# Kernel tuning notes

Measured on AMD Instinct MI355X. Metric: run time of the kernel, lower is better.

Reference implementation:

```python
import jax, jax.numpy as jnp
import numpy as np

HEADS = 4
DIM_HEAD = 32
SCALE = DIM_HEAD ** -0.5


def setup_inputs() -> dict:
    key = jax.random.key(0)
    k1, k2, k3 = jax.random.split(key, 3)
    B, C, H, W = 4, 128, 64, 64
    inner = HEADS * DIM_HEAD  # 128
    x = jax.random.normal(k1, (B, C, H, W), dtype=jnp.float32)
    # 1x1 conv weights == channel-mixing matrices [out_ch, in_ch]
    w_qkv = jax.random.normal(k2, (inner * 3, C), dtype=jnp.float32) * (C ** -0.5)
    w_proj = jax.random.normal(k3, (C, inner), dtype=jnp.float32) * (inner ** -0.5)
    b_proj = jnp.zeros((C,), dtype=jnp.float32)
    return {"x": x, "w_qkv": w_qkv, "w_proj": w_proj, "b_proj": b_proj}


def reference(x, w_qkv, w_proj, b_proj):
    b, c, h, w = x.shape
    n = h * w
    # 1x1 conv = per-pixel matmul over channels
    qkv = jnp.einsum('bchw,oc->bohw', x, w_qkv)  # [B, 3*inner, H, W]
    q, k, v = jnp.split(qkv, 3, axis=1)

    def to_heads(t):
        # [B, inner, H, W] -> [B, heads, HW, dim_head]
        return t.reshape(b, HEADS, DIM_HEAD, n).transpose(0, 1, 3, 2)

    q = to_heads(q) * SCALE
    k = to_heads(k)
    v = to_heads(v)
    # scores [B, heads, HW, HW]; softmax is max-stabilized (matches torch amax-subtract)
    scores = jnp.einsum('bhnd,bhmd->bhnm', q, k)
    attn = jax.nn.softmax(scores, axis=-1)
    out = jnp.einsum('bhnm,bhmd->bhnd', attn, v)  # [B, heads, HW, dim_head]
    out = out.transpose(0, 1, 3, 2).reshape(b, HEADS * DIM_HEAD, h, w)
    return jnp.einsum('bchw,oc->bohw', out, w_proj) + b_proj[None, :, None, None]
```

## Files before the change

### kernel.cpp

```cpp
#include <hip/hip_runtime.h>

typedef _Float16 f16;
typedef __attribute__((ext_vector_type(8))) f16 f16x8;
typedef __attribute__((ext_vector_type(4))) f16 f16x4;
typedef __attribute__((ext_vector_type(2))) __fp16 h16x2;
typedef __attribute__((ext_vector_type(4))) float floatx4;

#define NPIX 4096
#define KT   128
#define VROW 136
#define NSPLIT 4

__global__ __launch_bounds__(256) void cvt_w(
    const float* __restrict__ wq, const float* __restrict__ wp,
    f16* __restrict__ wh, f16* __restrict__ wph)
{
    const int idx = (blockIdx.x * 256 + threadIdx.x) * 4;
    const float qs = 0.17677669529663687f * 1.4426950408889634f;
    float4 v;
    f16* dst;
    if (idx < 49152) { v = *(const float4*)(wq + idx); dst = wh + idx; }
    else             { v = *(const float4*)(wp + (idx - 49152)); dst = wph + (idx - 49152); }
    if (idx < 16384) { v.x *= qs; v.y *= qs; v.z *= qs; v.w *= qs; }
    h16x2 a = __builtin_amdgcn_cvt_pkrtz(v.x, v.y);
    h16x2 b = __builtin_amdgcn_cvt_pkrtz(v.z, v.w);
    f16x4 h; h[0] = (f16)a[0]; h[1] = (f16)a[1]; h[2] = (f16)b[0]; h[3] = (f16)b[1];
    *(f16x4*)dst = h;
}

__global__ __launch_bounds__(256) void qkv_mfma(
    const float* __restrict__ x, const f16* __restrict__ wh,
    f16* __restrict__ qh, f16* __restrict__ kh, f16* __restrict__ vth)
{
    const int tid  = threadIdx.x;
    const int wave = tid >> 6;
    const int lane = tid & 63;
    const int quad = lane >> 4;
    const int l16  = lane & 15;
    const int pbase = blockIdx.x * 64;
    const int y     = blockIdx.y;
    const int b     = blockIdx.z;
    const int p_col = pbase + wave * 16 + l16;

    const float* xb = x + (size_t)b * 128 * NPIX;

    f16x8 xf[4];
#pragma unroll
    for (int kc = 0; kc < 4; ++kc) {
        const int c0 = kc * 32 + quad * 8;
        float e[8];
#pragma unroll
        for (int j = 0; j < 8; ++j)
            e[j] = xb[(size_t)(c0 + j) * NPIX + p_col];
#pragma unroll
        for (int j = 0; j < 4; ++j) {
            h16x2 pk = __builtin_amdgcn_cvt_pkrtz(e[2 * j], e[2 * j + 1]);
            xf[kc][2 * j] = (f16)pk[0]; xf[kc][2 * j + 1] = (f16)pk[1];
        }
    }

    floatx4 acc[4];
#pragma unroll
    for (int i = 0; i < 4; ++i) acc[i] = floatx4{0.f, 0.f, 0.f, 0.f};

    if (y < 4) {
#pragma unroll
        for (int n = 0; n < 4; ++n)
#pragma unroll
            for (int kc = 0; kc < 4; ++kc) {
                f16x8 wf = *(const f16x8*)&wh[(size_t)(y * 64 + n * 16 + l16) * 128 + kc * 32 + quad * 8];
                acc[n] = __builtin_amdgcn_mfma_f32_16x16x32_f16(xf[kc], wf, acc[n], 0, 0, 0);
            }
        f16* dst = (y < 2) ? qh : kh;
#pragma unroll
        for (int n = 0; n < 4; ++n) {
            const int og    = y * 64 + n * 16 + l16;
            const int local = og & 127;
            const int head  = local >> 5;
            const int d     = local & 31;
            f16* base = dst + (size_t)(b * 4 + head) * NPIX * 32;
#pragma unroll
            for (int r = 0; r < 4; ++r) {
                const int p = pbase + wave * 16 + quad * 4 + r;
                base[(size_t)p * 32 + d] = (f16)acc[n][r];
            }
        }
    } else {
#pragma unroll
        for (int m = 0; m < 4; ++m)
#pragma unroll
            for (int kc = 0; kc < 4; ++kc) {
                f16x8 wf = *(const f16x8*)&wh[(size_t)(y * 64 + m * 16 + l16) * 128 + kc * 32 + quad * 8];
                acc[m] = __builtin_amdgcn_mfma_f32_16x16x32_f16(wf, xf[kc], acc[m], 0, 0, 0);
            }
#pragma unroll
        for (int m = 0; m < 4; ++m)
#pragma unroll
            for (int r = 0; r < 4; ++r) {
                const int ov   = (y - 4) * 64 + m * 16 + quad * 4 + r;
                const int head = ov >> 5;
                const int d    = ov & 31;
                vth[((size_t)(b * 4 + head) * 32 + d) * NPIX + p_col] = (f16)acc[m][r];
            }
    }
}

__global__ __launch_bounds__(256, 4) void attn_kernel(
    const f16* __restrict__ qh, const f16* __restrict__ kh,
    const f16* __restrict__ vth, f16* __restrict__ po, float* __restrict__ pl)
{
    __shared__ f16 klds[KT * 32];
    __shared__ f16 vlds[32 * VROW];

    const int tid  = threadIdx.x;
    const int wave = tid >> 6;
    const int lane = tid & 63;
    const int quad = lane >> 4;
    const int l16  = lane & 15;

    const int n     = blockIdx.x;
    const int bh    = (n & 7) * 2 + ((n >> 3) & 1);
    const int qblk  = (n >> 4) & 31;
    const int split = (n >> 9) & 3;
    const int qbase = qblk * 128 + wave * 32;

    const f16* kb = kh + (size_t)bh * NPIX * 32;
    const f16* vb = vth + (size_t)bh * 32 * NPIX;

    f16x8 qB[2];
#pragma unroll
    for (int h = 0; h < 2; ++h)
        qB[h] = *(const f16x8*)(qh + ((size_t)bh * NPIX + qbase + h * 16 + l16) * 32 + quad * 8);

    f16x8 ones;
#pragma unroll
    for (int j = 0; j < 8; ++j) ones[j] = (l16 == 0) ? (f16)1.0f : (f16)0.0f;

    floatx4 oacc[2][2], lacc[2];
#pragma unroll
    for (int h = 0; h < 2; ++h) {
        lacc[h] = floatx4{0.f, 0.f, 0.f, 0.f};
#pragma unroll
        for (int dh = 0; dh < 2; ++dh) oacc[h][dh] = floatx4{0.f, 0.f, 0.f, 0.f};
    }

    for (int kt = split * 8; kt < split * 8 + 8; ++kt) {
        __syncthreads();
        {
            const int4* src = (const int4*)(kb + (size_t)kt * KT * 32);
            ((int4*)klds)[tid]       = src[tid];
            ((int4*)klds)[tid + 256] = src[tid + 256];
        }
        {
            const int r  = tid >> 3;
            const int cc = (tid & 7) * 2;
            const int4* vsrc = (const int4*)(vb + (size_t)r * NPIX + kt * KT + cc * 8);
            int4 v0 = vsrc[0], v1 = vsrc[1];
            int4* vdst = (int4*)(vlds + r * VROW + cc * 8);
            vdst[0] = v0; vdst[1] = v1;
        }
        __syncthreads();

        f16x8 kf[8];
#pragma unroll
        for (int t = 0; t < 8; ++t)
            kf[t] = *(const f16x8*)&klds[(t * 16 + l16) * 32 + quad * 8];

#pragma unroll
        for (int h = 0; h < 2; ++h) {
            floatx4 st[8];
            const floatx4 z0 = {0.f, 0.f, 0.f, 0.f};
#pragma unroll
            for (int t = 0; t < 8; ++t)
                st[t] = __builtin_amdgcn_mfma_f32_16x16x32_f16(kf[t], qB[h], z0, 0, 0, 0);

            f16x4 paf[8];
#pragma unroll
            for (int t = 0; t < 8; ++t) {
                float e0 = __builtin_amdgcn_exp2f(st[t][0]);
                float e1 = __builtin_amdgcn_exp2f(st[t][1]);
                float e2 = __builtin_amdgcn_exp2f(st[t][2]);
                float e3 = __builtin_amdgcn_exp2f(st[t][3]);
                h16x2 lo = __builtin_amdgcn_cvt_pkrtz(e0, e1);
                h16x2 hi = __builtin_amdgcn_cvt_pkrtz(e2, e3);
                paf[t][0] = (f16)lo[0]; paf[t][1] = (f16)lo[1];
                paf[t][2] = (f16)hi[0]; paf[t][3] = (f16)hi[1];
            }
#pragma unroll
            for (int g = 0; g < 4; ++g) {
                f16x8 pA;
#pragma unroll
                for (int j = 0; j < 4; ++j) { pA[j] = paf[2 * g][j]; pA[4 + j] = paf[2 * g + 1][j]; }
                lacc[h] = __builtin_amdgcn_mfma_f32_16x16x32_f16(pA, ones, lacc[h], 0, 0, 0);
#pragma unroll
                for (int dh = 0; dh < 2; ++dh) {
                    const f16* vrow = &vlds[(dh * 16 + l16) * VROW + 32 * g + quad * 4];
                    f16x4 v0 = *(const f16x4*)(vrow);
                    f16x4 v1 = *(const f16x4*)(vrow + 16);
                    f16x8 vB;
#pragma unroll
                    for (int j = 0; j < 4; ++j) { vB[j] = v0[j]; vB[4 + j] = v1[j]; }
                    oacc[h][dh] = __builtin_amdgcn_mfma_f32_16x16x32_f16(pA, vB, oacc[h][dh], 0, 0, 0);
                }
            }
        }
    }

    const size_t bq = (size_t)(split * 16 + bh) * NPIX;
#pragma unroll
    for (int h = 0; h < 2; ++h) {
        if (l16 == 0) {
#pragma unroll
            for (int r = 0; r < 4; ++r)
                pl[bq + qbase + h * 16 + quad * 4 + r] = lacc[h][r];
        }
        f16* poh = po + (bq + qbase + h * 16) * 32;
#pragma unroll
        for (int r = 0; r < 4; ++r) {
            poh[(quad * 4 + r) * 32 + l16]      = (f16)oacc[h][0][r];
            poh[(quad * 4 + r) * 32 + 16 + l16] = (f16)oacc[h][1][r];
        }
    }
}

__global__ __launch_bounds__(256) void proj_mfma(
    const f16* __restrict__ po, const float* __restrict__ pl,
    const f16* __restrict__ wph, const float* __restrict__ bp,
    float* __restrict__ out)
{
    const int tid  = threadIdx.x;
    const int wave = tid >> 6;
    const int lane = tid & 63;
    const int quad = lane >> 4;
    const int l16  = lane & 15;
    const int pbase = blockIdx.x * 64;
    const int obase = blockIdx.y * 64;
    const int b     = blockIdx.z;
    const int p_col = pbase + wave * 16 + l16;

    f16x8 bf[4];
#pragma unroll
    for (int kc = 0; kc < 4; ++kc) {
        const int bh = b * 4 + kc;
        float sums[8] = {0.f, 0.f, 0.f, 0.f, 0.f, 0.f, 0.f, 0.f};
        float lt = 0.f;
#pragma unroll
        for (int s = 0; s < NSPLIT; ++s) {
            const size_t bq = (size_t)(s * 16 + bh) * NPIX + p_col;
            f16x8 a = *(const f16x8*)(po + bq * 32 + quad * 8);
#pragma unroll
            for (int j = 0; j < 8; ++j) sums[j] += (float)a[j];
            lt += pl[bq];
        }
        const float inv = 1.0f / lt;
#pragma unroll
        for (int j = 0; j < 4; ++j) {
            h16x2 pk = __builtin_amdgcn_cvt_pkrtz(sums[2 * j] * inv, sums[2 * j + 1] * inv);
            bf[kc][2 * j] = (f16)pk[0]; bf[kc][2 * j + 1] = (f16)pk[1];
        }
    }

    floatx4 acc[4];
#pragma unroll
    for (int m = 0; m < 4; ++m) acc[m] = floatx4{0.f, 0.f, 0.f, 0.f};
#pragma unroll
    for (int m = 0; m < 4; ++m)
#pragma unroll
        for (int kc = 0; kc < 4; ++kc) {
            f16x8 af = *(const f16x8*)&wph[(size_t)(obase + m * 16 + l16) * 128 + kc * 32 + quad * 8];
            acc[m] = __builtin_amdgcn_mfma_f32_16x16x32_f16(af, bf[kc], acc[m], 0, 0, 0);
        }

#pragma unroll
    for (int m = 0; m < 4; ++m)
#pragma unroll
        for (int r = 0; r < 4; ++r) {
            const int o = obase + m * 16 + quad * 4 + r;
            out[((size_t)b * 128 + o) * NPIX + p_col] = acc[m][r] + bp[o];
        }
}

extern "C" void kernel_launch(void* const* d_in, const int* in_sizes, int n_in,
                              void* d_out, int out_size, void* d_ws, size_t ws_size,
                              hipStream_t stream)
{
    const float* x      = (const float*)d_in[0];
    const float* w_qkv  = (const float*)d_in[1];
    const float* w_proj = (const float*)d_in[2];
    const float* b_proj = (const float*)d_in[3];
    float* out = (float*)d_out;

    char* ws = (char*)d_ws;
    f16*   qh  = (f16*)(ws);
    f16*   kh  = (f16*)(ws + (4u << 20));
    f16*   vth = (f16*)(ws + (8u << 20));
    f16*   wh  = (f16*)(ws + (12u << 20));
    f16*   wph = (f16*)(ws + (12u << 20) + (96u << 10));
    float* pl  = (float*)(ws + (12u << 20) + (128u << 10));
    f16*   po  = (f16*)(ws + (13u << 20) + (128u << 10));

    cvt_w<<<dim3(64, 1, 1), 256, 0, stream>>>(w_qkv, w_proj, wh, wph);
    qkv_mfma<<<dim3(64, 6, 4), 256, 0, stream>>>(x, wh, qh, kh, vth);
    attn_kernel<<<dim3(2048, 1, 1), 256, 0, stream>>>(qh, kh, vth, po, pl);
    proj_mfma<<<dim3(64, 2, 4), 256, 0, stream>>>(po, pl, wph, b_proj, out);
}
```

Before: 141.5 us.

## Fuse weight conversion into GEMM kernels and stage tiles through LDS

Removes the separate cvt_w launch. The qkv and proj kernels now convert their fp32 weight slices to fp16 in shared memory themselves, with the q scaling applied per block. The qkv kernel also stages its x tile through LDS using coalesced float4 loads instead of strided scalar global loads. This saves one kernel launch and its round-trip through the workspace, but each block now repeats the conversion and pays an extra barrier and LDS footprint.

```diff
diff --git a/kernel.cpp b/kernel.cpp
--- a/kernel.cpp
+++ b/kernel.cpp
@@ -9,29 +9,16 @@
 #define NPIX 4096
 #define KT   128
 #define VROW 136
+#define XROW 66
 #define NSPLIT 4
 
-__global__ __launch_bounds__(256) void cvt_w(
-    const float* __restrict__ wq, const float* __restrict__ wp,
-    f16* __restrict__ wh, f16* __restrict__ wph)
-{
-    const int idx = (blockIdx.x * 256 + threadIdx.x) * 4;
-    const float qs = 0.17677669529663687f * 1.4426950408889634f;
-    float4 v;
-    f16* dst;
-    if (idx < 49152) { v = *(const float4*)(wq + idx); dst = wh + idx; }
-    else             { v = *(const float4*)(wp + (idx - 49152)); dst = wph + (idx - 49152); }
-    if (idx < 16384) { v.x *= qs; v.y *= qs; v.z *= qs; v.w *= qs; }
-    h16x2 a = __builtin_amdgcn_cvt_pkrtz(v.x, v.y);
-    h16x2 b = __builtin_amdgcn_cvt_pkrtz(v.z, v.w);
-    f16x4 h; h[0] = (f16)a[0]; h[1] = (f16)a[1]; h[2] = (f16)b[0]; h[3] = (f16)b[1];
-    *(f16x4*)dst = h;
-}
-
 __global__ __launch_bounds__(256) void qkv_mfma(
-    const float* __restrict__ x, const f16* __restrict__ wh,
+    const float* __restrict__ x, const float* __restrict__ wq,
     f16* __restrict__ qh, f16* __restrict__ kh, f16* __restrict__ vth)
 {
+    __shared__ float xlds[128 * XROW];
+    __shared__ f16   wlds[64 * 136];
+
     const int tid  = threadIdx.x;
     const int wave = tid >> 6;
     const int lane = tid & 63;
@@ -43,15 +30,36 @@
     const int p_col = pbase + wave * 16 + l16;
 
     const float* xb = x + (size_t)b * 128 * NPIX;
+    const float qs = (y < 2) ? 0.17677669529663687f * 1.4426950408889634f : 1.0f;
+
+#pragma unroll
+    for (int i = 0; i < 8; ++i) {
+        const int idx = i * 256 + tid;
+        const int o = idx >> 5, ch = idx & 31;
+        float4 wv = *(const float4*)(wq + (size_t)(y * 64 + o) * 128 + ch * 4);
+        h16x2 a = __builtin_amdgcn_cvt_pkrtz(wv.x * qs, wv.y * qs);
+        h16x2 c = __builtin_amdgcn_cvt_pkrtz(wv.z * qs, wv.w * qs);
+        f16x4 h; h[0] = (f16)a[0]; h[1] = (f16)a[1]; h[2] = (f16)c[0]; h[3] = (f16)c[1];
+        *(f16x4*)&wlds[o * 136 + ch * 4] = h;
+    }
+#pragma unroll
+    for (int i = 0; i < 8; ++i) {
+        const int idx = i * 256 + tid;
+        const int c = idx >> 4, p4 = (idx & 15) * 4;
+        float4 xv = *(const float4*)(xb + (size_t)c * NPIX + pbase + p4);
+        *(float4*)&xlds[c * XROW + p4] = xv;
+    }
+    __syncthreads();
 
     f16x8 xf[4];
 #pragma unroll
     for (int kc = 0; kc < 4; ++kc) {
         const int c0 = kc * 32 + quad * 8;
+        const int pl = wave * 16 + l16;
         float e[8];
 #pragma unroll
         for (int j = 0; j < 8; ++j)
-            e[j] = xb[(size_t)(c0 + j) * NPIX + p_col];
+            e[j] = xlds[(c0 + j) * XROW + pl];
 #pragma unroll
         for (int j = 0; j < 4; ++j) {
             h16x2 pk = __builtin_amdgcn_cvt_pkrtz(e[2 * j], e[2 * j + 1]);
@@ -68,7 +76,7 @@
         for (int n = 0; n < 4; ++n)
 #pragma unroll
             for (int kc = 0; kc < 4; ++kc) {
-                f16x8 wf = *(const f16x8*)&wh[(size_t)(y * 64 + n * 16 + l16) * 128 + kc * 32 + quad * 8];
+                f16x8 wf = *(const f16x8*)&wlds[(n * 16 + l16) * 136 + kc * 32 + quad * 8];
                 acc[n] = __builtin_amdgcn_mfma_f32_16x16x32_f16(xf[kc], wf, acc[n], 0, 0, 0);
             }
         f16* dst = (y < 2) ? qh : kh;
@@ -90,7 +98,7 @@
         for (int m = 0; m < 4; ++m)
 #pragma unroll
             for (int kc = 0; kc < 4; ++kc) {
-                f16x8 wf = *(const f16x8*)&wh[(size_t)(y * 64 + m * 16 + l16) * 128 + kc * 32 + quad * 8];
+                f16x8 wf = *(const f16x8*)&wlds[(m * 16 + l16) * 136 + kc * 32 + quad * 8];
                 acc[m] = __builtin_amdgcn_mfma_f32_16x16x32_f16(wf, xf[kc], acc[m], 0, 0, 0);
             }
 #pragma unroll
@@ -225,9 +233,10 @@
 
 __global__ __launch_bounds__(256) void proj_mfma(
     const f16* __restrict__ po, const float* __restrict__ pl,
-    const f16* __restrict__ wph, const float* __restrict__ bp,
+    const float* __restrict__ wp, const float* __restrict__ bp,
     float* __restrict__ out)
 {
+    __shared__ f16 wlds[64 * 136];
     const int tid  = threadIdx.x;
     const int wave = tid >> 6;
     const int lane = tid & 63;
@@ -238,6 +247,18 @@
     const int b     = blockIdx.z;
     const int p_col = pbase + wave * 16 + l16;
 
+#pragma unroll
+    for (int i = 0; i < 8; ++i) {
+        const int idx = i * 256 + tid;
+        const int o = idx >> 5, ch = idx & 31;
+        float4 wv = *(const float4*)(wp + (size_t)(obase + o) * 128 + ch * 4);
+        h16x2 a = __builtin_amdgcn_cvt_pkrtz(wv.x, wv.y);
+        h16x2 c = __builtin_amdgcn_cvt_pkrtz(wv.z, wv.w);
+        f16x4 h; h[0] = (f16)a[0]; h[1] = (f16)a[1]; h[2] = (f16)c[0]; h[3] = (f16)c[1];
+        *(f16x4*)&wlds[o * 136 + ch * 4] = h;
+    }
+    __syncthreads();
+
     f16x8 bf[4];
 #pragma unroll
     for (int kc = 0; kc < 4; ++kc) {
@@ -267,7 +288,7 @@
     for (int m = 0; m < 4; ++m)
 #pragma unroll
         for (int kc = 0; kc < 4; ++kc) {
-            f16x8 af = *(const f16x8*)&wph[(size_t)(obase + m * 16 + l16) * 128 + kc * 32 + quad * 8];
+            f16x8 af = *(const f16x8*)&wlds[(m * 16 + l16) * 136 + kc * 32 + quad * 8];
             acc[m] = __builtin_amdgcn_mfma_f32_16x16x32_f16(af, bf[kc], acc[m], 0, 0, 0);
         }
 
@@ -294,13 +315,10 @@
     f16*   qh  = (f16*)(ws);
     f16*   kh  = (f16*)(ws + (4u << 20));
     f16*   vth = (f16*)(ws + (8u << 20));
-    f16*   wh  = (f16*)(ws + (12u << 20));
-    f16*   wph = (f16*)(ws + (12u << 20) + (96u << 10));
-    float* pl  = (float*)(ws + (12u << 20) + (128u << 10));
-    f16*   po  = (f16*)(ws + (13u << 20) + (128u << 10));
-
-    cvt_w<<<dim3(64, 1, 1), 256, 0, stream>>>(w_qkv, w_proj, wh, wph);
-    qkv_mfma<<<dim3(64, 6, 4), 256, 0, stream>>>(x, wh, qh, kh, vth);
+    float* pl  = (float*)(ws + (12u << 20));
+    f16*   po  = (f16*)(ws + (13u << 20));
+
+    qkv_mfma<<<dim3(64, 6, 4), 256, 0, stream>>>(x, w_qkv, qh, kh, vth);
     attn_kernel<<<dim3(2048, 1, 1), 256, 0, stream>>>(qh, kh, vth, po, pl);
-    proj_mfma<<<dim3(64, 2, 4), 256, 0, stream>>>(po, pl, wph, b_proj, out);
+    proj_mfma<<<dim3(64, 2, 4), 256, 0, stream>>>(po, pl, w_proj, b_proj, out);
 }
```

New measurement: 132.0 us. -6.7%, faster.
